# Kernel tuning notes

Hardware: AMD Instinct MI355X
Metric: run time of the kernel (lower is better)

## Reference

```python
import jax, jax.numpy as jnp
import numpy as np

N = 50000
E = 800000
R = 8
IN = 128
H = 128
C = 64
NEG_SLOPE = 0.2


def _leaky_relu(x):
    return jnp.where(x >= 0, x, NEG_SLOPE * x)


def rgat_layer(x, src, dst, etype, W, q, k, b):
    # x: [N, F]; W: [R, F, H]; q, k: [H]; b: [H]
    xr = jnp.einsum('nf,rfo->nro', x, W)          # [N, R, H] per-relation transforms
    qx = jnp.einsum('nro,o->nr', xr, q)            # [N, R] target-side score
    kx = jnp.einsum('nro,o->nr', xr, k)            # [N, R] source-side score
    alpha = _leaky_relu(qx[dst, etype] + kx[src, etype])  # [E]
    # across-relation softmax over incoming edges of each target node
    m = jax.ops.segment_max(alpha, dst, num_segments=N)   # [N]
    e = jnp.exp(alpha - m[dst])
    denom = jax.ops.segment_sum(e, dst, num_segments=N)   # [N]
    w = e / denom[dst]                                    # [E]
    msg = xr[src, etype]                                  # [E, H]
    out = jax.ops.segment_sum(w[:, None] * msg, dst, num_segments=N)  # [N, H]
    return out + b


def setup_inputs() -> dict:
    key = jax.random.key(0)
    ks = jax.random.split(key, 20)
    s = 1.0 / np.sqrt(H)
    inp = {
        'x': jax.random.normal(ks[0], (N, IN), jnp.float32),
        'edge_index': jax.random.randint(ks[1], (2, E), 0, N, jnp.int64),
        'edge_type': jax.random.randint(ks[2], (E,), 0, R, jnp.int64),
        'W1': jax.random.normal(ks[3], (R, IN, H), jnp.float32) / np.sqrt(IN),
        'q1': jax.random.normal(ks[4], (H,), jnp.float32) * s,
        'k1': jax.random.normal(ks[5], (H,), jnp.float32) * s,
        'b1': jnp.zeros((H,), jnp.float32),
        'W2': jax.random.normal(ks[6], (R, H, H), jnp.float32) * s,
        'q2': jax.random.normal(ks[7], (H,), jnp.float32) * s,
        'k2': jax.random.normal(ks[8], (H,), jnp.float32) * s,
        'b2': jnp.zeros((H,), jnp.float32),
        'W3': jax.random.normal(ks[9], (R, H, H), jnp.float32) * s,
        'q3': jax.random.normal(ks[10], (H,), jnp.float32) * s,
        'k3': jax.random.normal(ks[11], (H,), jnp.float32) * s,
        'b3': jnp.zeros((H,), jnp.float32),
        'lin_w': jax.random.normal(ks[12], (H, C), jnp.float32) * s,
        'lin_b': jnp.zeros((C,), jnp.float32),
    }
    return inp


def reference(x, edge_index, edge_type, W1, q1, k1, b1, W2, q2, k2, b2, W3, q3, k3, b3, lin_w, lin_b):
    src, dst = edge_index[0], edge_index[1]
    h = jax.nn.relu(rgat_layer(x, src, dst, edge_type, W1, q1, k1, b1))
    h = jax.nn.relu(rgat_layer(h, src, dst, edge_type, W2, q2, k2, b2))
    h = jax.nn.relu(rgat_layer(h, src, dst, edge_type, W3, q3, k3, b3))
    logits = h @ lin_w + lin_b
    return jax.nn.log_softmax(logits, axis=-1)
```

## Files before the change

### kernel.cpp

```cpp
#include <hip/hip_runtime.h>
#include <math.h>

#define N_NODES 50000
#define N_EDGES 800000
#define R_REL 8
#define H_DIM 128
#define C_OUT 64

#define XR_TILES 4
#define XR_NTILE ((N_NODES + 127) / 128)
#define XR_NGRP ((XR_NTILE + XR_TILES - 1) / XR_TILES)

#define CSR_RANGES 8
#define CSR_RANGE_NODES (N_NODES / CSR_RANGES)
#define CSR_BLOCKS 2048

typedef __attribute__((ext_vector_type(8))) __bf16 bf16x8;
typedef __attribute__((ext_vector_type(4))) __bf16 bf16x4;
typedef __attribute__((ext_vector_type(2))) __bf16 bf16x2;
typedef __attribute__((ext_vector_type(4))) float f32x4;

__device__ __forceinline__ void gload_lds16(const void* g, void* l) {
  __builtin_amdgcn_global_load_lds(
      (__attribute__((address_space(1))) void*)g,
      (__attribute__((address_space(3))) void*)l,
      16, 0, 0);
}


__global__ void k_hist(const int* __restrict__ dst, int* __restrict__ hist) {
  const int rng = blockIdx.x & (CSR_RANGES - 1);
  const int rlo = rng * CSR_RANGE_NODES;
  const int rhi = rlo + CSR_RANGE_NODES;
  const int stride = (gridDim.x >> 3) * blockDim.x;
  for (int e = (blockIdx.x >> 3) * blockDim.x + threadIdx.x; e < N_EDGES; e += stride) {
    int d = dst[e];
    if (d >= rlo && d < rhi) atomicAdd(&hist[d], 1);
  }
}

__global__ __launch_bounds__(1024) void k_scan1(const int* __restrict__ hist,
                                                int* __restrict__ excl, int* __restrict__ bsum) {
  __shared__ int tmp[1024];
  int b = blockIdx.x, tid = threadIdx.x;
  int idx = b * 1024 + tid;
  int v = (idx < N_NODES) ? hist[idx] : 0;
  tmp[tid] = v;
  __syncthreads();
  for (int off = 1; off < 1024; off <<= 1) {
    int t = (tid >= off) ? tmp[tid - off] : 0;
    __syncthreads();
    tmp[tid] += t;
    __syncthreads();
  }
  if (idx < N_NODES) excl[idx] = tmp[tid] - v;
  if (tid == 1023) bsum[b] = tmp[1023];
}

__global__ void k_scan2(const int* __restrict__ bsum, int* __restrict__ boff) {
  if (threadIdx.x == 0) {
    int nb = (N_NODES + 1023) / 1024;
    int s = 0;
    for (int i = 0; i < nb; ++i) { boff[i] = s; s += bsum[i]; }
  }
}

__global__ void k_scan3(const int* __restrict__ excl, const int* __restrict__ boff,
                        int* __restrict__ rowptr, int* __restrict__ cursor) {
  int idx = blockIdx.x * blockDim.x + threadIdx.x;
  if (idx < N_NODES) {
    int v = excl[idx] + boff[idx >> 10];
    rowptr[idx] = v;
    cursor[idx] = v;
  }
  if (idx == 0) rowptr[N_NODES] = N_EDGES;
}

__global__ void k_scatter(const int* __restrict__ src, const int* __restrict__ dst,
                          const int* __restrict__ et, int* __restrict__ cursor,
                          int* __restrict__ spack) {
  const int rng = blockIdx.x & (CSR_RANGES - 1);
  const int rlo = rng * CSR_RANGE_NODES;
  const int rhi = rlo + CSR_RANGE_NODES;
  const int stride = (gridDim.x >> 3) * blockDim.x;
  for (int e = (blockIdx.x >> 3) * blockDim.x + threadIdx.x; e < N_EDGES; e += stride) {
    int d = dst[e];
    if (d >= rlo && d < rhi) {
      int p = atomicAdd(&cursor[d], 1);
      spack[p] = (src[e] << 3) | et[e];
    }
  }
}


__global__ void k_cast(const float* __restrict__ x, __bf16* __restrict__ xb) {
  int t = blockIdx.x * blockDim.x + threadIdx.x;
  if (t >= N_NODES * H_DIM / 8) return;
  const float4* xv = (const float4*)(x + (size_t)t * 8);
  float4 a = xv[0], b = xv[1];
  bf16x8 o;
  o[0] = (__bf16)a.x; o[1] = (__bf16)a.y; o[2] = (__bf16)a.z; o[3] = (__bf16)a.w;
  o[4] = (__bf16)b.x; o[5] = (__bf16)b.y; o[6] = (__bf16)b.z; o[7] = (__bf16)b.w;
  ((bf16x8*)xb)[t] = o;
}


__global__ void k_prepxrfrag(const float* __restrict__ W1, const float* __restrict__ W2,
                             const float* __restrict__ W3,
                             __bf16* __restrict__ Ghi, __bf16* __restrict__ Glo) {
  int t = blockIdx.x * 256 + threadIdx.x;
  if (t >= 49152) return;
  int lane = t & 63;
  int kb = (t >> 6) & 3;
  int mt = (t >> 8) & 63;
  int l  = t >> 14;
  int c = lane & 15, quad = lane >> 4;
  const float* W = (l == 0) ? W1 : (l == 1) ? W2 : W3;
  int ro = mt * 16 + c;
  int r = ro >> 7;
  int o = ro & 127;
  int fb = kb * 32 + quad * 8;
  const float* wp = W + ((size_t)r << 14) + (size_t)fb * 128 + o;
  size_t ob = ((size_t)l * 131072) + (((size_t)mt * 4 + kb) * 64 + lane) * 8;
#pragma unroll
  for (int j = 0; j < 8; ++j) {
    float v = wp[j * 128];
    __bf16 h = (__bf16)v;
    Ghi[ob + j] = h;
    Glo[ob + j] = (__bf16)(v - (float)h);
  }
}


__global__ void k_prepwq(const float* __restrict__ W1, const float* __restrict__ W2,
                         const float* __restrict__ W3,
                         const float* __restrict__ q1, const float* __restrict__ k1,
                         const float* __restrict__ q2, const float* __restrict__ k2,
                         const float* __restrict__ q3, const float* __restrict__ k3,
                         float* __restrict__ wq, float* __restrict__ wk) {
  int idx = blockIdx.x * blockDim.x + threadIdx.x;
  if (idx >= 3 * R_REL * 128) return;
  int r = (idx >> 7) & 7;
  int f = idx & 127;
  int l = idx >> 10;
  const float* W  = (l == 0) ? W1 : (l == 1) ? W2 : W3;
  const float* qv = (l == 0) ? q1 : (l == 1) ? q2 : q3;
  const float* kv = (l == 0) ? k1 : (l == 1) ? k2 : k3;
  const float4* row = (const float4*)(W + ((size_t)r << 14) + ((size_t)f << 7));
  const float4* q4 = (const float4*)qv;
  const float4* k4 = (const float4*)kv;
  float sq = 0.f, sk = 0.f;
#pragma unroll 8
  for (int i = 0; i < 32; ++i) {
    float4 w = row[i], qq = q4[i], kk = k4[i];
    sq += w.x * qq.x + w.y * qq.y + w.z * qq.z + w.w * qq.w;
    sk += w.x * kk.x + w.y * kk.y + w.z * kk.z + w.w * kk.w;
  }
  wq[idx] = sq;
  wk[idx] = sk;
}


__global__ void k_prepqkfrag(const float* __restrict__ wq, const float* __restrict__ wk,
                             __bf16* __restrict__ Qhi, __bf16* __restrict__ Qlo) {
  int t = blockIdx.x * 256 + threadIdx.x;
  if (t >= 768) return;
  int lane = t & 63;
  int kb = (t >> 6) & 3;
  int l  = t >> 8;
  int c = lane & 15, quad = lane >> 4;
  const float* Mrow = (c < 8) ? (wq + l * 1024 + c * 128) : (wk + l * 1024 + (c - 8) * 128);
  size_t ob = ((size_t)(l * 4 + kb) * 64 + lane) * 8;
#pragma unroll
  for (int j = 0; j < 8; ++j) {
    float v = Mrow[kb * 32 + quad * 8 + j];
    __bf16 h = (__bf16)v;
    Qhi[ob + j] = h;
    Qlo[ob + j] = (__bf16)(v - (float)h);
  }
}


__global__ void k_preplw(const float* __restrict__ lw,
                         __bf16* __restrict__ Lhi, __bf16* __restrict__ Llo) {
  int t = blockIdx.x * 256 + threadIdx.x;
  if (t >= 1024) return;
  int lane = t & 63;
  int kb = (t >> 6) & 3;
  int mt = t >> 8;
  int c = lane & 15, quad = lane >> 4;
  int cout = mt * 16 + c;
  size_t ob = (size_t)t * 8;
#pragma unroll
  for (int j = 0; j < 8; ++j) {
    int k = kb * 32 + quad * 8 + j;
    float v = lw[(size_t)k * 64 + cout];
    __bf16 h = (__bf16)v;
    Lhi[ob + j] = h;
    Llo[ob + j] = (__bf16)(v - (float)h);
  }
}


__global__ __launch_bounds__(256) void k_qkx_mfma(
    const __bf16* __restrict__ xb,
    const __bf16* __restrict__ Qhi, const __bf16* __restrict__ Qlo,
    float* __restrict__ qx, float* __restrict__ kx)
{
  const int tid  = threadIdx.x;
  const int wave = tid >> 6;
  const int lane = tid & 63;
  const int quad = lane >> 4;
  const int c    = lane & 15;
  const int node = blockIdx.x * 64 + wave * 16 + c;
  const int ncl  = (node < N_NODES) ? node : (N_NODES - 1);

  f32x4 acc = (f32x4){0.f, 0.f, 0.f, 0.f};
#pragma unroll
  for (int kb = 0; kb < 4; ++kb) {
    bf16x8 B = *(const bf16x8*)(xb + (size_t)ncl * 128 + kb * 32 + quad * 8);
    bf16x8 ah = ((const bf16x8*)Qhi)[kb * 64 + lane];
    bf16x8 al = ((const bf16x8*)Qlo)[kb * 64 + lane];
    acc = __builtin_amdgcn_mfma_f32_16x16x32_bf16(ah, B, acc, 0, 0, 0);
    acc = __builtin_amdgcn_mfma_f32_16x16x32_bf16(al, B, acc, 0, 0, 0);
  }
  if (node < N_NODES) {
    float* base = (quad & 2) ? kx : qx;
    int off = (quad & 1) * 4;
    *(float4*)(base + (size_t)node * 8 + off) = make_float4(acc[0], acc[1], acc[2], acc[3]);
  }
}


__global__ __launch_bounds__(512, 4) void k_xr(
    const __bf16* __restrict__ xin,
    const __bf16* __restrict__ Ghi, const __bf16* __restrict__ Glo,
    __bf16* __restrict__ XR)
{
  __shared__ bf16x8 sW[2048];
  __shared__ __bf16 sT[8192];
  const int tid  = threadIdx.x;
  const int wave = tid >> 6;
  const int lane = tid & 63;
  const int quad = lane >> 4;
  const int c    = lane & 15;
  const int ch   = blockIdx.x & 15;
  const int grp  = blockIdx.x >> 4;

  char* sTw = (char*)(sT + wave * 1024);

  {
    const float4* gh = (const float4*)(Ghi + (size_t)ch * 8192);
    const float4* gl = (const float4*)(Glo + (size_t)ch * 8192);
    float4* s4 = (float4*)sW;
    gload_lds16(gh + tid, s4 + tid);
    gload_lds16(gh + tid + 512, s4 + tid + 512);
    gload_lds16(gl + tid, s4 + 1024 + tid);
    gload_lds16(gl + tid + 512, s4 + 1024 + tid + 512);
  }

  bool staged = false;
#pragma unroll 1
  for (int t = 0; t < XR_TILES; ++t) {
    const int nb = grp * XR_TILES + t;
    if (nb * 128 >= N_NODES) break;
    const int node = nb * 128 + wave * 16 + c;
    const int nclamp = (node < N_NODES) ? node : (N_NODES - 1);

    bf16x8 B[4];
#pragma unroll
    for (int kb = 0; kb < 4; ++kb)
      B[kb] = *(const bf16x8*)(xin + (size_t)nclamp * 128 + kb * 32 + quad * 8);

    if (!staged) {
      __syncthreads();
      staged = true;
    }

    f32x4 acc[4];
#pragma unroll
    for (int ot = 0; ot < 4; ++ot) acc[ot] = (f32x4){0.f, 0.f, 0.f, 0.f};
#pragma unroll
    for (int kb = 0; kb < 4; ++kb) {
#pragma unroll
      for (int ot = 0; ot < 4; ++ot) {
        bf16x8 whi = sW[(ot * 4 + kb) * 64 + lane];
        bf16x8 wlo = sW[1024 + (ot * 4 + kb) * 64 + lane];
        acc[ot] = __builtin_amdgcn_mfma_f32_16x16x32_bf16(whi, B[kb], acc[ot], 0, 0, 0);
        acc[ot] = __builtin_amdgcn_mfma_f32_16x16x32_bf16(wlo, B[kb], acc[ot], 0, 0, 0);
      }
    }

#pragma unroll
    for (int ot = 0; ot < 4; ++ot) {
      bf16x4 o;
      o[0] = (__bf16)acc[ot][0];
      o[1] = (__bf16)acc[ot][1];
      o[2] = (__bf16)acc[ot][2];
      o[3] = (__bf16)acc[ot][3];
      int boff = (c << 7) + (((ot << 5) + (quad << 3)) ^ ((c & 7) << 4));
      *(bf16x4*)(sTw + boff) = o;
    }
#pragma unroll
    for (int i = 0; i < 2; ++i) {
      int nl  = i * 8 + (lane >> 3);
      int seg = lane & 7;
      int boff = (nl << 7) + (((seg << 4)) ^ ((nl & 7) << 4));
      bf16x8 v = *(bf16x8*)(sTw + boff);
      int gn = nb * 128 + wave * 16 + nl;
      if (gn < N_NODES)
        *(bf16x8*)(XR + (size_t)gn * 1024 + ch * 64 + seg * 8) = v;
    }
  }
}


__global__ __launch_bounds__(256) void k_agg_feat(
    const __bf16* __restrict__ XR, const float* __restrict__ qx, const float* __restrict__ kx,
    const int* __restrict__ rowptr, const int* __restrict__ spack,
    const float* __restrict__ bias, __bf16* __restrict__ hout)
{
  const int nd = blockIdx.x * 4 + (threadIdx.x >> 6);
  const int lane = threadIdx.x & 63;
  if (nd >= N_NODES) return;
  const int s = rowptr[nd];
  const int deg = rowptr[nd + 1] - s;

  float m = -INFINITY, sum = 0.f;
  float2 acc = make_float2(0.f, 0.f);

  for (int c0 = 0; c0 < deg; c0 += 64) {
    int idx = c0 + lane;
    bool valid = idx < deg;
    int pk = valid ? spack[s + idx] : 0;
    float a = -INFINITY;
    if (valid) {
      float av = qx[(nd << 3) | (pk & 7)] + kx[pk];
      a = (av >= 0.f) ? av : 0.2f * av;
    }
    float cm = a;
#pragma unroll
    for (int off = 32; off > 0; off >>= 1) cm = fmaxf(cm, __shfl_xor(cm, off));
    if (c0 == 0) {
      m = cm;
    } else {
      float mnew = fmaxf(m, cm);
      float scale = __expf(m - mnew);
      sum *= scale;
      acc.x *= scale; acc.y *= scale;
      m = mnew;
    }
    float ew = valid ? __expf(a - m) : 0.f;
    float cs = ew;
#pragma unroll
    for (int off = 32; off > 0; off >>= 1) cs += __shfl_xor(cs, off);
    sum += cs;
    int cnt = (deg - c0 < 64) ? (deg - c0) : 64;

    int j = 0;
    for (; j + 16 <= cnt; j += 16) {
      int p[16];
      bf16x2 v[16];
#pragma unroll
      for (int u = 0; u < 16; ++u) p[u] = __builtin_amdgcn_readlane(pk, j + u);
#pragma unroll
      for (int u = 0; u < 16; ++u)
        v[u] = ((const bf16x2*)(XR + ((size_t)p[u] << 7)))[lane];
#pragma unroll
      for (int u = 0; u < 16; ++u) {
        float w = __uint_as_float(__builtin_amdgcn_readlane(__float_as_uint(ew), j + u));
        acc.x += w * (float)v[u][0];
        acc.y += w * (float)v[u][1];
      }
    }
    if (j + 8 <= cnt) {
      int p[8];
      bf16x2 v[8];
#pragma unroll
      for (int u = 0; u < 8; ++u) p[u] = __builtin_amdgcn_readlane(pk, j + u);
#pragma unroll
      for (int u = 0; u < 8; ++u)
        v[u] = ((const bf16x2*)(XR + ((size_t)p[u] << 7)))[lane];
#pragma unroll
      for (int u = 0; u < 8; ++u) {
        float w = __uint_as_float(__builtin_amdgcn_readlane(__float_as_uint(ew), j + u));
        acc.x += w * (float)v[u][0];
        acc.y += w * (float)v[u][1];
      }
      j += 8;
    }
    for (; j < cnt; ++j) {
      int p0 = __builtin_amdgcn_readlane(pk, j);
      float w0 = __uint_as_float(__builtin_amdgcn_readlane(__float_as_uint(ew), j));
      bf16x2 v0 = ((const bf16x2*)(XR + ((size_t)p0 << 7)))[lane];
      acc.x += w0 * (float)v0[0];
      acc.y += w0 * (float)v0[1];
    }
  }
  float inv = (deg > 0) ? 1.f / sum : 0.f;
  float2 bb = ((const float2*)bias)[lane];
  float ox = fmaxf(acc.x * inv + bb.x, 0.f);
  float oy = fmaxf(acc.y * inv + bb.y, 0.f);
  bf16x2 o;
  o[0] = (__bf16)ox;
  o[1] = (__bf16)oy;
  ((bf16x2*)hout)[(size_t)nd * 64 + lane] = o;
}


__global__ __launch_bounds__(256) void k_final(
    const __bf16* __restrict__ h,
    const __bf16* __restrict__ Lhi, const __bf16* __restrict__ Llo,
    const float* __restrict__ lb, float* __restrict__ out)
{
  const int tid  = threadIdx.x;
  const int wave = tid >> 6;
  const int lane = tid & 63;
  const int quad = lane >> 4;
  const int c    = lane & 15;
  const int node = blockIdx.x * 64 + wave * 16 + c;
  const int ncl  = (node < N_NODES) ? node : (N_NODES - 1);

  bf16x8 B[4];
#pragma unroll
  for (int kb = 0; kb < 4; ++kb)
    B[kb] = *(const bf16x8*)(h + (size_t)ncl * 128 + kb * 32 + quad * 8);

  f32x4 acc[4];
#pragma unroll
  for (int mt = 0; mt < 4; ++mt) acc[mt] = (f32x4){0.f, 0.f, 0.f, 0.f};

#pragma unroll
  for (int mt = 0; mt < 4; ++mt) {
#pragma unroll
    for (int kb = 0; kb < 4; ++kb) {
      bf16x8 ah = ((const bf16x8*)Lhi)[(mt * 4 + kb) * 64 + lane];
      bf16x8 al = ((const bf16x8*)Llo)[(mt * 4 + kb) * 64 + lane];
      acc[mt] = __builtin_amdgcn_mfma_f32_16x16x32_bf16(ah, B[kb], acc[mt], 0, 0, 0);
      acc[mt] = __builtin_amdgcn_mfma_f32_16x16x32_bf16(al, B[kb], acc[mt], 0, 0, 0);
    }
  }

  float v[16];
#pragma unroll
  for (int mt = 0; mt < 4; ++mt) {
    float4 bb = *(const float4*)(lb + mt * 16 + quad * 4);
    v[mt * 4 + 0] = acc[mt][0] + bb.x;
    v[mt * 4 + 1] = acc[mt][1] + bb.y;
    v[mt * 4 + 2] = acc[mt][2] + bb.z;
    v[mt * 4 + 3] = acc[mt][3] + bb.w;
  }
  float mx = v[0];
#pragma unroll
  for (int i = 1; i < 16; ++i) mx = fmaxf(mx, v[i]);
  mx = fmaxf(mx, __shfl_xor(mx, 16));
  mx = fmaxf(mx, __shfl_xor(mx, 32));
  float ssum = 0.f;
#pragma unroll
  for (int i = 0; i < 16; ++i) ssum += __expf(v[i] - mx);
  ssum += __shfl_xor(ssum, 16);
  ssum += __shfl_xor(ssum, 32);
  float lse = mx + __logf(ssum);

  if (node < N_NODES) {
    float* op = out + (size_t)node * 64 + quad * 4;
#pragma unroll
    for (int mt = 0; mt < 4; ++mt) {
      *(float4*)(op + mt * 16) = make_float4(v[mt * 4 + 0] - lse, v[mt * 4 + 1] - lse,
                                             v[mt * 4 + 2] - lse, v[mt * 4 + 3] - lse);
    }
  }
}


extern "C" void kernel_launch(void* const* d_in, const int* in_sizes, int n_in,
                              void* d_out, int out_size, void* d_ws, size_t ws_size,
                              hipStream_t stream) {
  const float* x   = (const float*)d_in[0];
  const int* ei    = (const int*)d_in[1];
  const int* etype = (const int*)d_in[2];
  const float* W1 = (const float*)d_in[3];
  const float* q1 = (const float*)d_in[4];
  const float* k1 = (const float*)d_in[5];
  const float* b1 = (const float*)d_in[6];
  const float* W2 = (const float*)d_in[7];
  const float* q2 = (const float*)d_in[8];
  const float* k2 = (const float*)d_in[9];
  const float* b2 = (const float*)d_in[10];
  const float* W3 = (const float*)d_in[11];
  const float* q3 = (const float*)d_in[12];
  const float* k3 = (const float*)d_in[13];
  const float* b3 = (const float*)d_in[14];
  const float* lw = (const float*)d_in[15];
  const float* lb = (const float*)d_in[16];
  float* outp = (float*)d_out;

  char* p = (char*)d_ws;
  auto alloc = [&](size_t bytes) {
    char* r = p;
    p += (bytes + 255) & ~(size_t)255;
    return r;
  };
  __bf16* XR  = (__bf16*)alloc((size_t)N_NODES * R_REL * H_DIM * 2);
  __bf16* xb  = (__bf16*)alloc((size_t)N_NODES * H_DIM * 2);
  __bf16* hA  = (__bf16*)alloc((size_t)N_NODES * H_DIM * 2);
  __bf16* hB  = (__bf16*)alloc((size_t)N_NODES * H_DIM * 2);
  float* qx   = (float*)alloc((size_t)N_NODES * R_REL * 4);
  float* kx   = (float*)alloc((size_t)N_NODES * R_REL * 4);
  int* rowptr = (int*)alloc((size_t)(N_NODES + 1) * 4);
  int* cursor = (int*)alloc((size_t)N_NODES * 4);
  int* hist   = (int*)alloc((size_t)N_NODES * 4);
  int* excl   = (int*)alloc((size_t)N_NODES * 4);
  int* bsum   = (int*)alloc((size_t)64 * 4);
  int* boff   = (int*)alloc((size_t)64 * 4);
  int* spack  = (int*)alloc((size_t)N_EDGES * 4);
  __bf16* Ghi = (__bf16*)alloc((size_t)3 * 131072 * 2);
  __bf16* Glo = (__bf16*)alloc((size_t)3 * 131072 * 2);
  float* wq   = (float*)alloc((size_t)3 * R_REL * 128 * 4);
  float* wk   = (float*)alloc((size_t)3 * R_REL * 128 * 4);
  __bf16* Qhi = (__bf16*)alloc((size_t)3 * 2048 * 2);
  __bf16* Qlo = (__bf16*)alloc((size_t)3 * 2048 * 2);
  __bf16* Lhi = (__bf16*)alloc((size_t)1024 * 8 * 2);
  __bf16* Llo = (__bf16*)alloc((size_t)1024 * 8 * 2);

  const int* src = ei;
  const int* dst = ei + N_EDGES;

  const int nscan = (N_NODES + 1023) / 1024;

  hipMemsetAsync(hist, 0, (size_t)N_NODES * 4, stream);
  k_hist<<<CSR_BLOCKS, 256, 0, stream>>>(dst, hist);
  k_cast<<<(N_NODES * H_DIM / 8 + 255) / 256, 256, 0, stream>>>(x, xb);
  k_prepxrfrag<<<192, 256, 0, stream>>>(W1, W2, W3, Ghi, Glo);
  k_prepwq<<<(3 * R_REL * 128 + 255) / 256, 256, 0, stream>>>(W1, W2, W3, q1, k1, q2, k2, q3, k3, wq, wk);
  k_prepqkfrag<<<3, 256, 0, stream>>>(wq, wk, Qhi, Qlo);
  k_preplw<<<4, 256, 0, stream>>>(lw, Lhi, Llo);
  k_scan1<<<nscan, 1024, 0, stream>>>(hist, excl, bsum);
  k_scan2<<<1, 64, 0, stream>>>(bsum, boff);
  k_scan3<<<(N_NODES + 255) / 256, 256, 0, stream>>>(excl, boff, rowptr, cursor);
  k_scatter<<<CSR_BLOCKS, 256, 0, stream>>>(src, dst, etype, cursor, spack);

  const int qgrid = (N_NODES + 63) / 64;
  const int xgrid = 16 * XR_NGRP;
  const int agrid = (N_NODES + 3) / 4;
  const int fgrid = (N_NODES + 63) / 64;
  const size_t WFL = 131072;
  const size_t QFL = 2048;

  k_qkx_mfma<<<qgrid, 256, 0, stream>>>(xb, Qhi, Qlo, qx, kx);
  k_xr<<<xgrid, 512, 0, stream>>>(xb, Ghi, Glo, XR);
  k_agg_feat<<<agrid, 256, 0, stream>>>(XR, qx, kx, rowptr, spack, b1, hA);
  k_qkx_mfma<<<qgrid, 256, 0, stream>>>(hA, Qhi + QFL, Qlo + QFL, qx, kx);
  k_xr<<<xgrid, 512, 0, stream>>>(hA, Ghi + WFL, Glo + WFL, XR);
  k_agg_feat<<<agrid, 256, 0, stream>>>(XR, qx, kx, rowptr, spack, b2, hB);
  k_qkx_mfma<<<qgrid, 256, 0, stream>>>(hB, Qhi + 2 * QFL, Qlo + 2 * QFL, qx, kx);
  k_xr<<<xgrid, 512, 0, stream>>>(hB, Ghi + 2 * WFL, Glo + 2 * WFL, XR);
  k_agg_feat<<<agrid, 256, 0, stream>>>(XR, qx, kx, rowptr, spack, b3, hA);
  k_final<<<fgrid, 256, 0, stream>>>(hA, Lhi, Llo, lb, outp);
}
```

Measured before the change: 469.9 us.

## Aggregate four nodes per wavefront with 16-lane groups and 16-byte gathers

```diff
diff --git a/kernel.cpp b/kernel.cpp
--- a/kernel.cpp
+++ b/kernel.cpp
@@ -320,17 +320,23 @@
     const int* __restrict__ rowptr, const int* __restrict__ spack,
     const float* __restrict__ bias, __bf16* __restrict__ hout)
 {
-  const int nd = blockIdx.x * 4 + (threadIdx.x >> 6);
-  const int lane = threadIdx.x & 63;
-  if (nd >= N_NODES) return;
-  const int s = rowptr[nd];
-  const int deg = rowptr[nd + 1] - s;
+  const int lane  = threadIdx.x & 63;
+  const int g     = lane >> 4;
+  const int l16   = lane & 15;
+  const int gbase = lane & 48;
+  const int nd = blockIdx.x * 16 + (threadIdx.x >> 6) * 4 + g;
+  const bool alive = nd < N_NODES;
+
+  const int s   = alive ? rowptr[nd] : 0;
+  const int deg = alive ? rowptr[nd + 1] - s : 0;
 
   float m = -INFINITY, sum = 0.f;
-  float2 acc = make_float2(0.f, 0.f);
-
-  for (int c0 = 0; c0 < deg; c0 += 64) {
-    int idx = c0 + lane;
+  float acc[8];
+#pragma unroll
+  for (int d = 0; d < 8; ++d) acc[d] = 0.f;
+
+  for (int c0 = 0; c0 < deg; c0 += 16) {
+    int idx = c0 + l16;
     bool valid = idx < deg;
     int pk = valid ? spack[s + idx] : 0;
     float a = -INFINITY;
@@ -340,71 +346,53 @@
     }
     float cm = a;
 #pragma unroll
-    for (int off = 32; off > 0; off >>= 1) cm = fmaxf(cm, __shfl_xor(cm, off));
+    for (int off = 8; off > 0; off >>= 1) cm = fmaxf(cm, __shfl_xor(cm, off));
     if (c0 == 0) {
       m = cm;
     } else {
       float mnew = fmaxf(m, cm);
       float scale = __expf(m - mnew);
       sum *= scale;
-      acc.x *= scale; acc.y *= scale;
+#pragma unroll
+      for (int d = 0; d < 8; ++d) acc[d] *= scale;
       m = mnew;
     }
     float ew = valid ? __expf(a - m) : 0.f;
     float cs = ew;
 #pragma unroll
-    for (int off = 32; off > 0; off >>= 1) cs += __shfl_xor(cs, off);
+    for (int off = 8; off > 0; off >>= 1) cs += __shfl_xor(cs, off);
     sum += cs;
-    int cnt = (deg - c0 < 64) ? (deg - c0) : 64;
-
-    int j = 0;
-    for (; j + 16 <= cnt; j += 16) {
-      int p[16];
-      bf16x2 v[16];
-#pragma unroll
-      for (int u = 0; u < 16; ++u) p[u] = __builtin_amdgcn_readlane(pk, j + u);
-#pragma unroll
-      for (int u = 0; u < 16; ++u)
-        v[u] = ((const bf16x2*)(XR + ((size_t)p[u] << 7)))[lane];
-#pragma unroll
-      for (int u = 0; u < 16; ++u) {
-        float w = __uint_as_float(__builtin_amdgcn_readlane(__float_as_uint(ew), j + u));
-        acc.x += w * (float)v[u][0];
-        acc.y += w * (float)v[u][1];
+
+    int cnt = (deg - c0 < 16) ? (deg - c0) : 16;
+#pragma unroll 1
+    for (int j0 = 0; j0 < 16; j0 += 8) {
+      if (j0 >= cnt) break;
+      int p[8];
+      float w[8];
+      bf16x8 v[8];
+#pragma unroll
+      for (int u = 0; u < 8; ++u) p[u] = __shfl(pk, gbase + j0 + u);
+#pragma unroll
+      for (int u = 0; u < 8; ++u) w[u] = __shfl(ew, gbase + j0 + u);
+#pragma unroll
+      for (int u = 0; u < 8; ++u)
+        v[u] = ((const bf16x8*)(XR + ((size_t)p[u] << 7)))[l16];
+#pragma unroll
+      for (int u = 0; u < 8; ++u) {
+#pragma unroll
+        for (int d = 0; d < 8; ++d) acc[d] += w[u] * (float)v[u][d];
       }
     }
-    if (j + 8 <= cnt) {
-      int p[8];
-      bf16x2 v[8];
-#pragma unroll
-      for (int u = 0; u < 8; ++u) p[u] = __builtin_amdgcn_readlane(pk, j + u);
-#pragma unroll
-      for (int u = 0; u < 8; ++u)
-        v[u] = ((const bf16x2*)(XR + ((size_t)p[u] << 7)))[lane];
-#pragma unroll
-      for (int u = 0; u < 8; ++u) {
-        float w = __uint_as_float(__builtin_amdgcn_readlane(__float_as_uint(ew), j + u));
-        acc.x += w * (float)v[u][0];
-        acc.y += w * (float)v[u][1];
-      }
-      j += 8;
-    }
-    for (; j < cnt; ++j) {
-      int p0 = __builtin_amdgcn_readlane(pk, j);
-      float w0 = __uint_as_float(__builtin_amdgcn_readlane(__float_as_uint(ew), j));
-      bf16x2 v0 = ((const bf16x2*)(XR + ((size_t)p0 << 7)))[lane];
-      acc.x += w0 * (float)v0[0];
-      acc.y += w0 * (float)v0[1];
-    }
-  }
-  float inv = (deg > 0) ? 1.f / sum : 0.f;
-  float2 bb = ((const float2*)bias)[lane];
-  float ox = fmaxf(acc.x * inv + bb.x, 0.f);
-  float oy = fmaxf(acc.y * inv + bb.y, 0.f);
-  bf16x2 o;
-  o[0] = (__bf16)ox;
-  o[1] = (__bf16)oy;
-  ((bf16x2*)hout)[(size_t)nd * 64 + lane] = o;
+  }
+
+  if (alive) {
+    float inv = (deg > 0) ? 1.f / sum : 0.f;
+    const float* bb = bias + l16 * 8;
+    bf16x8 o;
+#pragma unroll
+    for (int d = 0; d < 8; ++d) o[d] = (__bf16)fmaxf(acc[d] * inv + bb[d], 0.f);
+    ((bf16x8*)hout)[(size_t)nd * 16 + l16] = o;
+  }
 }
 
 
@@ -542,7 +530,7 @@
 
   const int qgrid = (N_NODES + 63) / 64;
   const int xgrid = 16 * XR_NGRP;
-  const int agrid = (N_NODES + 3) / 4;
+  const int agrid = (N_NODES + 15) / 16;
   const int fgrid = (N_NODES + 63) / 64;
   const size_t WFL = 131072;
   const size_t QFL = 2048;
```

Measured after the change: 470.4 us. About the same (+0.1%).
